# Kernel tuning notes

Hardware: AMD Instinct MI355X
Metric: run time of the kernel (lower is better)

The kernel has to match this reference:

```python
import jax, jax.numpy as jnp
import numpy as np

IN_F = 4096
OUT_F = 4096
N = 16384


def setup_inputs() -> dict:
    key = jax.random.key(0)
    kx, kw = jax.random.split(key)
    x = jax.random.normal(kx, (N, IN_F), dtype=jnp.float32)
    # reset_parameters: weight ~ N(0, 1/in_features), bias = 0
    weight = jax.random.normal(kw, (OUT_F, IN_F), dtype=jnp.float32) * (1.0 / np.sqrt(IN_F))
    bias = jnp.zeros((OUT_F,), dtype=jnp.float32)
    return {"x": x, "weight": weight, "bias": bias}


def reference(x, weight, bias):
    # binary_linear_scalar: per-output-row scaling factor alpha = mean(|W|),
    # binarized weight bw = sign(W) * alpha  (XNOR-Net style)
    alpha = jnp.mean(jnp.abs(weight), axis=1, keepdims=True)  # [out, 1]
    bw = jnp.sign(weight) * alpha                             # [out, in]
    # y = x @ bw^T + bias
    return jnp.einsum('ni,oi->no', x, bw) + bias
```

## Files before the change

### kernel.cpp

```cpp
#include <hip/hip_runtime.h>
#include <hip/hip_bf16.h>
#include <stdint.h>

#define IN_F  4096
#define OUT_F 4096
#define NROWS 16384
#define NT    (IN_F / 64)

typedef unsigned short u16;
typedef unsigned int u32;
typedef unsigned long long u64;
typedef __bf16 bf16x8 __attribute__((ext_vector_type(8)));
typedef float  f32x4  __attribute__((ext_vector_type(4)));
typedef u16    u16x8  __attribute__((ext_vector_type(8)));

#define BAR()   asm volatile("s_barrier" ::: "memory")
#define LGKM0() asm volatile("s_waitcnt lgkmcnt(0)" ::: "memory")
#define VM4()   asm volatile("s_waitcnt vmcnt(4)" ::: "memory")
#define VM0()   asm volatile("s_waitcnt vmcnt(0)" ::: "memory")

__device__ __forceinline__ u16 f2bf(float x) {
    union { float f; uint32_t u; } c; c.f = x;
    uint32_t u = c.u;
    return (u16)((u + 0x7FFFu + ((u >> 16) & 1u)) >> 16);
}

__device__ __forceinline__ void gload_lds16(const void* g, void* l) {
    __builtin_amdgcn_global_load_lds(
        (const __attribute__((address_space(1))) void*)g,
        (__attribute__((address_space(3))) void*)l, 16, 0, 0);
}

__device__ __forceinline__ u16 sgn_bf16(float v) {
    return v > 0.f ? 0x3F80 : (v < 0.f ? 0xBF80 : 0);
}

__global__ void prep_wbits_kernel(const float* __restrict__ W,
                                  float* __restrict__ alpha,
                                  u64* __restrict__ Wbits) {
    const int row = blockIdx.x;
    const int wave = threadIdx.x >> 6, lane = threadIdx.x & 63;
    const float* wr = W + (size_t)row * IN_F;
    float s = 0.f;
#pragma unroll 4
    for (int it = 0; it < 16; ++it) {
        const int kword = it * 4 + wave;
        float v = __builtin_nontemporal_load(wr + kword * 64 + lane);
        s += fabsf(v);
        u64 m = __ballot(v > 0.f);
        if (lane == 0) Wbits[(size_t)kword * OUT_F + row] = m;
    }
    for (int off = 32; off > 0; off >>= 1) s += __shfl_down(s, off);
    __shared__ float red[4];
    if (lane == 0) red[wave] = s;
    __syncthreads();
    if (threadIdx.x == 0)
        alpha[row] = (red[0] + red[1] + red[2] + red[3]) * (1.0f / IN_F);
}

__global__ void convx_kernel(const float* __restrict__ X, u16* __restrict__ O,
                             int swz) {
    const size_t idx = (size_t)blockIdx.x * 256 + threadIdx.x;
    const int row = (int)(idx >> 9);
    const int q = (int)idx & 511;
    const int g = q >> 3, c8 = q & 7;
    const int c8s = swz ? (c8 ^ (row & 7)) : c8;
    const f32x4* src = reinterpret_cast<const f32x4*>(
        X + (size_t)row * IN_F + g * 64 + c8s * 8);
    f32x4 a = __builtin_nontemporal_load(src);
    f32x4 b = __builtin_nontemporal_load(src + 1);
    u16x8 r;
    r[0] = f2bf(a[0]); r[1] = f2bf(a[1]); r[2] = f2bf(a[2]); r[3] = f2bf(a[3]);
    r[4] = f2bf(b[0]); r[5] = f2bf(b[1]); r[6] = f2bf(b[2]); r[7] = f2bf(b[3]);
    reinterpret_cast<u16x8*>(O)[idx] = r;
}

__global__ __launch_bounds__(512, 2) void gemm8_kernel(
    const u16* __restrict__ Xbf, const u64* __restrict__ Wbits,
    const float* __restrict__ alpha, const float* __restrict__ bias,
    float* __restrict__ Y) {
    __shared__ u16 Alds[3][16384];
    __shared__ u16 Blds[2][16384];

    const int tid  = threadIdx.x;
    const int lane = tid & 63, wave = tid >> 6;
    const int wm = wave >> 2, wn = wave & 3;
    const int lrow = lane & 15;

    const int wg = blockIdx.x;
    const int i  = wg >> 3;
    const int m0 = (((wg & 7) << 3) | (i >> 4)) << 8;
    const int n0 = (i & 15) << 8;

    const int q0 = ((lane >> 4) << 3) ^ ((lrow & 7) << 3);
    const int q1 = q0 ^ 32;

    const int erow = tid >> 1, ehalf = tid & 1;
    const u32* Wb32 = reinterpret_cast<const u32*>(Wbits);

    f32x4 acc[8][4];
#pragma unroll
    for (int a = 0; a < 8; ++a)
#pragma unroll
        for (int b = 0; b < 4; ++b) acc[a][b] = (f32x4){0.f, 0.f, 0.f, 0.f};

    auto stageA = [&](int th, int half, u16* buf) {
        if (th >= NT) return;
#pragma unroll
        for (int t2 = 0; t2 < 2; ++t2) {
            const int c = half * 1024 + t2 * 512 + tid;
            const int row = c >> 3, c8 = c & 7;
            gload_lds16(Xbf + (size_t)(m0 + row) * IN_F + th * 64 + c8 * 8,
                        buf + c * 8);
        }
    };

    auto expandB = [&](unsigned b, int dstbuf, int jlo) {
        unsigned nb = ~b;
        u16* base = &Blds[dstbuf][erow * 64];
#pragma unroll
        for (int j = 0; j < 2; ++j) {
            const int jj = jlo + j;
            const int k8 = 4 * ehalf + jj;
            union { unsigned u[4]; u16x8 v; } r;
#pragma unroll
            for (int e = 0; e < 4; ++e) {
                unsigned s = nb >> (jj * 8 + 2 * e);
                r.u[e] = 0x3F803F80u | ((s & 1u) << 15) | ((s & 2u) << 30);
            }
            *reinterpret_cast<u16x8*>(base + ((k8 ^ (erow & 7)) << 3)) = r.v;
        }
    };

    u16* pa0 = &Alds[0][0];
    u16* pa1 = &Alds[1][0];
    u16* pa2 = &Alds[2][0];

    unsigned b0 = Wb32[(size_t)(n0 + erow) * 2 + ehalf];
    stageA(0, 0, pa0); stageA(0, 1, pa0);
    unsigned bits_cur = Wb32[(size_t)8192 + (n0 + erow) * 2 + ehalf];
    stageA(1, 0, pa1); stageA(1, 1, pa1);
    unsigned bits_nxt = 0;
    expandB(b0, 0, 0); expandB(b0, 0, 2);
    VM4();
    LGKM0(); BAR();

    for (int t = 0; t < NT; ++t) {
        const u16* Ar = pa0 + wm * 8192 + lrow * 64;
        const u16* Br = &Blds[t & 1][0] + wn * 4096 + lrow * 64;
        bf16x8 bfr[4][2];

#pragma unroll
        for (int nf = 0; nf < 4; ++nf) {
            bfr[nf][0] = *reinterpret_cast<const bf16x8*>(Br + nf * 1024 + q0);
            bfr[nf][1] = *reinterpret_cast<const bf16x8*>(Br + nf * 1024 + q1);
        }
        if (t + 2 < NT)
            bits_nxt = Wb32[(size_t)(t + 2) * 8192 + (n0 + erow) * 2 + ehalf];

        bf16x8 aP0 = *reinterpret_cast<const bf16x8*>(Ar + q0);
        bf16x8 aP1 = *reinterpret_cast<const bf16x8*>(Ar + q1);
#pragma unroll
        for (int mm = 0; mm < 8; ++mm) {
            bf16x8 aQ0, aQ1;
            if (mm < 7) {
                aQ0 = *reinterpret_cast<const bf16x8*>(Ar + (mm + 1) * 1024 + q0);
                aQ1 = *reinterpret_cast<const bf16x8*>(Ar + (mm + 1) * 1024 + q1);
            }
            if (mm == 1) stageA(t + 2, 0, pa2);
            if (mm == 3 && t + 1 < NT) expandB(bits_cur, (t + 1) & 1, 0);
            if (mm == 4) stageA(t + 2, 1, pa2);
            if (mm == 5 && t + 1 < NT) expandB(bits_cur, (t + 1) & 1, 2);

            __builtin_amdgcn_s_setprio(1);
#pragma unroll
            for (int nn = 0; nn < 4; ++nn) {
                acc[mm][nn] = __builtin_amdgcn_mfma_f32_16x16x32_bf16(aP0, bfr[nn][0], acc[mm][nn], 0, 0, 0);
                acc[mm][nn] = __builtin_amdgcn_mfma_f32_16x16x32_bf16(aP1, bfr[nn][1], acc[mm][nn], 0, 0, 0);
            }
            __builtin_amdgcn_s_setprio(0);
            aP0 = aQ0; aP1 = aQ1;
        }

        if (t >= NT - 2) { VM0(); } else { VM4(); }
        LGKM0(); BAR();

        bits_cur = bits_nxt;
        u16* tp = pa0; pa0 = pa1; pa1 = pa2; pa2 = tp;
    }

#pragma unroll
    for (int nf = 0; nf < 4; ++nf) {
        const int col = n0 + wn * 64 + nf * 16 + lrow;
        const float al = alpha[col], bi = bias[col];
#pragma unroll
        for (int mf = 0; mf < 8; ++mf) {
            const int rbase = m0 + wm * 128 + mf * 16 + ((lane >> 4) << 2);
#pragma unroll
            for (int r = 0; r < 4; ++r)
                __builtin_nontemporal_store(acc[mf][nf][r] * al + bi,
                    &Y[(size_t)(rbase + r) * OUT_F + col]);
        }
    }
}

__global__ void prep_w_kernel(const float* __restrict__ W,
                              float* __restrict__ alpha,
                              u16* __restrict__ S) {
    const int row = blockIdx.x;
    const float* wr = W + (size_t)row * IN_F;
    float s = 0.f;
    for (int c = threadIdx.x; c < 512; c += 256) {
        const f32x4* src = reinterpret_cast<const f32x4*>(wr + c * 8);
        f32x4 v0 = __builtin_nontemporal_load(src);
        f32x4 v1 = __builtin_nontemporal_load(src + 1);
        s += fabsf(v0[0]) + fabsf(v0[1]) + fabsf(v0[2]) + fabsf(v0[3])
           + fabsf(v1[0]) + fabsf(v1[1]) + fabsf(v1[2]) + fabsf(v1[3]);
        u16x8 r;
        r[0] = sgn_bf16(v0[0]); r[1] = sgn_bf16(v0[1]);
        r[2] = sgn_bf16(v0[2]); r[3] = sgn_bf16(v0[3]);
        r[4] = sgn_bf16(v1[0]); r[5] = sgn_bf16(v1[1]);
        r[6] = sgn_bf16(v1[2]); r[7] = sgn_bf16(v1[3]);
        *reinterpret_cast<u16x8*>(S + (size_t)row * IN_F + c * 8) = r;
    }
    for (int off = 32; off > 0; off >>= 1) s += __shfl_down(s, off);
    __shared__ float red[4];
    const int wave = threadIdx.x >> 6, lane = threadIdx.x & 63;
    if (lane == 0) red[wave] = s;
    __syncthreads();
    if (threadIdx.x == 0)
        alpha[row] = (red[0] + red[1] + red[2] + red[3]) * (1.0f / IN_F);
}

__global__ __launch_bounds__(256) void gemm_fallback(
    const float* __restrict__ X, const u16* __restrict__ Wsign,
    const float* __restrict__ alpha, const float* __restrict__ bias,
    float* __restrict__ Y) {
    __shared__ u16 Axl[128 * 64];
    __shared__ u16 Bxl[128 * 64];

    const int tid = threadIdx.x;
    const int n0 = blockIdx.x * 128;
    const int m0 = blockIdx.y * 128;
    const int wave = tid >> 6, lane = tid & 63;
    const int wm = wave >> 1, wn = wave & 1;
    const int lrow = lane & 15;
    const int lk8 = (lane >> 4) * 8;

    f32x4 acc[4][4];
#pragma unroll
    for (int a = 0; a < 4; ++a)
#pragma unroll
        for (int b = 0; b < 4; ++b) acc[a][b] = (f32x4){0.f, 0.f, 0.f, 0.f};

    for (int kt = 0; kt < IN_F; kt += 64) {
#pragma unroll
        for (int j = 0; j < 4; ++j) {
            const int idx = j * 256 + tid;
            const int row = idx >> 3, c8 = idx & 7;
            gload_lds16(Wsign + (size_t)(n0 + row) * IN_F + kt + c8 * 8,
                        &Bxl[idx * 8]);
        }
#pragma unroll
        for (int j = 0; j < 4; ++j) {
            const int idx = j * 256 + tid;
            const int row = idx >> 3, c8 = idx & 7;
            const float* src = X + (size_t)(m0 + row) * IN_F + kt + c8 * 8;
            float4 v0 = *reinterpret_cast<const float4*>(src);
            float4 v1 = *reinterpret_cast<const float4*>(src + 4);
            u16x8 r;
            r[0] = f2bf(v0.x); r[1] = f2bf(v0.y); r[2] = f2bf(v0.z); r[3] = f2bf(v0.w);
            r[4] = f2bf(v1.x); r[5] = f2bf(v1.y); r[6] = f2bf(v1.z); r[7] = f2bf(v1.w);
            *reinterpret_cast<u16x8*>(&Axl[idx * 8]) = r;
        }
        __syncthreads();
#pragma unroll
        for (int kk = 0; kk < 2; ++kk) {
            bf16x8 af[4], bfv[4];
#pragma unroll
            for (int mf = 0; mf < 4; ++mf)
                af[mf] = *reinterpret_cast<const bf16x8*>(
                    &Axl[(wm * 64 + mf * 16 + lrow) * 64 + kk * 32 + lk8]);
#pragma unroll
            for (int nf = 0; nf < 4; ++nf)
                bfv[nf] = *reinterpret_cast<const bf16x8*>(
                    &Bxl[(wn * 64 + nf * 16 + lrow) * 64 + kk * 32 + lk8]);
#pragma unroll
            for (int mf = 0; mf < 4; ++mf)
#pragma unroll
                for (int nf = 0; nf < 4; ++nf)
                    acc[mf][nf] = __builtin_amdgcn_mfma_f32_16x16x32_bf16(
                        af[mf], bfv[nf], acc[mf][nf], 0, 0, 0);
        }
        __syncthreads();
    }
#pragma unroll
    for (int nf = 0; nf < 4; ++nf) {
        const int col = n0 + wn * 64 + nf * 16 + lrow;
        const float al = alpha[col], bi = bias[col];
#pragma unroll
        for (int mf = 0; mf < 4; ++mf) {
            const int rbase = m0 + wm * 64 + mf * 16 + (lane >> 4) * 4;
#pragma unroll
            for (int r = 0; r < 4; ++r)
                __builtin_nontemporal_store(acc[mf][nf][r] * al + bi,
                    &Y[(size_t)(rbase + r) * OUT_F + col]);
        }
    }
}

extern "C" void kernel_launch(void* const* d_in, const int* in_sizes, int n_in,
                              void* d_out, int out_size, void* d_ws, size_t ws_size,
                              hipStream_t stream) {
    const float* X    = (const float*)d_in[0];
    const float* W    = (const float*)d_in[1];
    const float* bias = (const float*)d_in[2];
    float* Y = (float*)d_out;

    char* ws = (char*)d_ws;
    float* alpha = (float*)ws;
    const size_t WBITS_OFF = 16384;
    const size_t XBF_OFF   = WBITS_OFF + (size_t)OUT_F * (IN_F / 8);
    const size_t need_fast = XBF_OFF + (size_t)NROWS * IN_F * 2;

    if (ws_size >= need_fast) {
        u64* Wbits = (u64*)(ws + WBITS_OFF);
        u16* Xbf   = (u16*)(ws + XBF_OFF);
        prep_wbits_kernel<<<OUT_F, 256, 0, stream>>>(W, alpha, Wbits);
        convx_kernel<<<(size_t)NROWS * IN_F / 8 / 256, 256, 0, stream>>>(X, Xbf, 1);
        gemm8_kernel<<<dim3(1024), 512, 0, stream>>>(Xbf, Wbits, alpha, bias, Y);
    } else {
        u16* Wsign = (u16*)(ws + 16384);
        prep_w_kernel<<<OUT_F, 256, 0, stream>>>(W, alpha, Wsign);
        dim3 grid(OUT_F / 128, NROWS / 128);
        gemm_fallback<<<grid, 256, 0, stream>>>(X, Wsign, alpha, bias, Y);
    }
}
```

Before: 514.3 us.

## Expand binarized weight bits directly into MFMA B registers, drop B LDS staging

The kernel no longer expands sign bits into a double-buffered LDS B tile and reads it back. Each wave now loads its own u64 bit words from global memory and expands them in registers into bf16 MFMA operands, one 16-column fragment at a time. All A fragments for a k-tile are read up front, and the MFMA loop is reordered column-fragment-major. This removes LDS writes and reads for B, frees 64KB of LDS, and drops the explicit vmcnt/lgkmcnt waits. The risks are higher register pressure and possible races on the asynchronous LDS-direct A loads, since only a barrier remains.

```diff
diff --git a/kernel.cpp b/kernel.cpp
--- a/kernel.cpp
+++ b/kernel.cpp
@@ -15,9 +15,7 @@
 typedef u16    u16x8  __attribute__((ext_vector_type(8)));
 
 #define BAR()   asm volatile("s_barrier" ::: "memory")
-#define LGKM0() asm volatile("s_waitcnt lgkmcnt(0)" ::: "memory")
 #define VM4()   asm volatile("s_waitcnt vmcnt(4)" ::: "memory")
-#define VM0()   asm volatile("s_waitcnt vmcnt(0)" ::: "memory")
 
 __device__ __forceinline__ u16 f2bf(float x) {
     union { float f; uint32_t u; } c; c.f = x;
@@ -80,7 +78,6 @@
     const float* __restrict__ alpha, const float* __restrict__ bias,
     float* __restrict__ Y) {
     __shared__ u16 Alds[3][16384];
-    __shared__ u16 Blds[2][16384];
 
     const int tid  = threadIdx.x;
     const int lane = tid & 63, wave = tid >> 6;
@@ -94,9 +91,8 @@
 
     const int q0 = ((lane >> 4) << 3) ^ ((lrow & 7) << 3);
     const int q1 = q0 ^ 32;
-
-    const int erow = tid >> 1, ehalf = tid & 1;
-    const u32* Wb32 = reinterpret_cast<const u32*>(Wbits);
+    const int sh = (lane >> 4) << 3;
+    const int brow = n0 + wn * 64 + lrow;
 
     f32x4 acc[8][4];
 #pragma unroll
@@ -115,77 +111,84 @@
         }
     };
 
-    auto expandB = [&](unsigned b, int dstbuf, int jlo) {
-        unsigned nb = ~b;
-        u16* base = &Blds[dstbuf][erow * 64];
-#pragma unroll
-        for (int j = 0; j < 2; ++j) {
-            const int jj = jlo + j;
-            const int k8 = 4 * ehalf + jj;
-            union { unsigned u[4]; u16x8 v; } r;
-#pragma unroll
-            for (int e = 0; e < 4; ++e) {
-                unsigned s = nb >> (jj * 8 + 2 * e);
-                r.u[e] = 0x3F803F80u | ((s & 1u) << 15) | ((s & 2u) << 30);
-            }
-            *reinterpret_cast<u16x8*>(base + ((k8 ^ (erow & 7)) << 3)) = r.v;
-        }
+    u64 wcur[4];
+    auto loadbits = [&](int th) {
+        if (th >= NT) return;
+#pragma unroll
+        for (int nf = 0; nf < 4; ++nf)
+            wcur[nf] = Wbits[(size_t)th * OUT_F + brow + nf * 16];
+    };
+
+    auto expand_pair = [&](u64 w, bf16x8* dst) {
+        u64 t64 = w >> sh;
+        unsigned nb0 = ~(unsigned)t64;
+        unsigned nb1 = ~(unsigned)(t64 >> 32);
+        union { unsigned u[4]; bf16x8 v; } r0, r1;
+#pragma unroll
+        for (int e = 0; e < 4; ++e) {
+            unsigned s0 = nb0 >> (2 * e), s1 = nb1 >> (2 * e);
+            r0.u[e] = 0x3F803F80u | ((s0 & 1u) << 15) | ((s0 & 2u) << 30);
+            r1.u[e] = 0x3F803F80u | ((s1 & 1u) << 15) | ((s1 & 2u) << 30);
+        }
+        dst[0] = r0.v; dst[1] = r1.v;
     };
 
     u16* pa0 = &Alds[0][0];
     u16* pa1 = &Alds[1][0];
     u16* pa2 = &Alds[2][0];
 
-    unsigned b0 = Wb32[(size_t)(n0 + erow) * 2 + ehalf];
     stageA(0, 0, pa0); stageA(0, 1, pa0);
-    unsigned bits_cur = Wb32[(size_t)8192 + (n0 + erow) * 2 + ehalf];
     stageA(1, 0, pa1); stageA(1, 1, pa1);
-    unsigned bits_nxt = 0;
-    expandB(b0, 0, 0); expandB(b0, 0, 2);
-    VM4();
-    LGKM0(); BAR();
+    loadbits(0);
+    VM4(); BAR();
 
     for (int t = 0; t < NT; ++t) {
         const u16* Ar = pa0 + wm * 8192 + lrow * 64;
-        const u16* Br = &Blds[t & 1][0] + wn * 4096 + lrow * 64;
-        bf16x8 bfr[4][2];
-
-#pragma unroll
-        for (int nf = 0; nf < 4; ++nf) {
-            bfr[nf][0] = *reinterpret_cast<const bf16x8*>(Br + nf * 1024 + q0);
-            bfr[nf][1] = *reinterpret_cast<const bf16x8*>(Br + nf * 1024 + q1);
-        }
-        if (t + 2 < NT)
-            bits_nxt = Wb32[(size_t)(t + 2) * 8192 + (n0 + erow) * 2 + ehalf];
-
-        bf16x8 aP0 = *reinterpret_cast<const bf16x8*>(Ar + q0);
-        bf16x8 aP1 = *reinterpret_cast<const bf16x8*>(Ar + q1);
-#pragma unroll
-        for (int mm = 0; mm < 8; ++mm) {
-            bf16x8 aQ0, aQ1;
-            if (mm < 7) {
-                aQ0 = *reinterpret_cast<const bf16x8*>(Ar + (mm + 1) * 1024 + q0);
-                aQ1 = *reinterpret_cast<const bf16x8*>(Ar + (mm + 1) * 1024 + q1);
-            }
-            if (mm == 1) stageA(t + 2, 0, pa2);
-            if (mm == 3 && t + 1 < NT) expandB(bits_cur, (t + 1) & 1, 0);
-            if (mm == 4) stageA(t + 2, 1, pa2);
-            if (mm == 5 && t + 1 < NT) expandB(bits_cur, (t + 1) & 1, 2);
-
-            __builtin_amdgcn_s_setprio(1);
-#pragma unroll
-            for (int nn = 0; nn < 4; ++nn) {
-                acc[mm][nn] = __builtin_amdgcn_mfma_f32_16x16x32_bf16(aP0, bfr[nn][0], acc[mm][nn], 0, 0, 0);
-                acc[mm][nn] = __builtin_amdgcn_mfma_f32_16x16x32_bf16(aP1, bfr[nn][1], acc[mm][nn], 0, 0, 0);
-            }
-            __builtin_amdgcn_s_setprio(0);
-            aP0 = aQ0; aP1 = aQ1;
-        }
-
-        if (t >= NT - 2) { VM0(); } else { VM4(); }
-        LGKM0(); BAR();
-
-        bits_cur = bits_nxt;
+        bf16x8 af0[8], af1[8];
+#pragma unroll
+        for (int mm = 0; mm < 8; ++mm) {
+            af0[mm] = *reinterpret_cast<const bf16x8*>(Ar + mm * 1024 + q0);
+            af1[mm] = *reinterpret_cast<const bf16x8*>(Ar + mm * 1024 + q1);
+        }
+
+        bf16x8 bP[2], bQ[2];
+        expand_pair(wcur[0], bP);
+        __builtin_amdgcn_s_setprio(1);
+#pragma unroll
+        for (int mm = 0; mm < 8; ++mm) {
+            acc[mm][0] = __builtin_amdgcn_mfma_f32_16x16x32_bf16(af0[mm], bP[0], acc[mm][0], 0, 0, 0);
+            acc[mm][0] = __builtin_amdgcn_mfma_f32_16x16x32_bf16(af1[mm], bP[1], acc[mm][0], 0, 0, 0);
+        }
+        __builtin_amdgcn_s_setprio(0);
+        expand_pair(wcur[1], bQ);
+        stageA(t + 2, 0, pa2); stageA(t + 2, 1, pa2);
+        __builtin_amdgcn_s_setprio(1);
+#pragma unroll
+        for (int mm = 0; mm < 8; ++mm) {
+            acc[mm][1] = __builtin_amdgcn_mfma_f32_16x16x32_bf16(af0[mm], bQ[0], acc[mm][1], 0, 0, 0);
+            acc[mm][1] = __builtin_amdgcn_mfma_f32_16x16x32_bf16(af1[mm], bQ[1], acc[mm][1], 0, 0, 0);
+        }
+        __builtin_amdgcn_s_setprio(0);
+        expand_pair(wcur[2], bP);
+        __builtin_amdgcn_s_setprio(1);
+#pragma unroll
+        for (int mm = 0; mm < 8; ++mm) {
+            acc[mm][2] = __builtin_amdgcn_mfma_f32_16x16x32_bf16(af0[mm], bP[0], acc[mm][2], 0, 0, 0);
+            acc[mm][2] = __builtin_amdgcn_mfma_f32_16x16x32_bf16(af1[mm], bP[1], acc[mm][2], 0, 0, 0);
+        }
+        __builtin_amdgcn_s_setprio(0);
+        expand_pair(wcur[3], bQ);
+        loadbits(t + 1);
+        __builtin_amdgcn_s_setprio(1);
+#pragma unroll
+        for (int mm = 0; mm < 8; ++mm) {
+            acc[mm][3] = __builtin_amdgcn_mfma_f32_16x16x32_bf16(af0[mm], bQ[0], acc[mm][3], 0, 0, 0);
+            acc[mm][3] = __builtin_amdgcn_mfma_f32_16x16x32_bf16(af1[mm], bQ[1], acc[mm][3], 0, 0, 0);
+        }
+        __builtin_amdgcn_s_setprio(0);
+
+        BAR();
+
         u16* tp = pa0; pa0 = pa1; pa1 = pa2; pa2 = tp;
     }
 
```

After: 524.7 us. 2.0% more time.
